# Performance work log

Hardware: AMD Instinct MI355X
Metric: run time of the kernel (lower is better)

## Reference

```python
import jax, jax.numpy as jnp
import numpy as np

S = 8192      # total patch tokens
NSEG = 8      # number of images/segments (equal length)
D = 1280      # embed dim
H = 16        # heads
HD = 80       # head dim
MLP = 3456    # swiglu hidden


def setup_inputs() -> dict:
    key = jax.random.key(0)
    ks = jax.random.split(key, 8)
    def w(k, shape):
        return jax.random.normal(k, shape, jnp.float32) * 0.02
    return {
        "x": jax.random.normal(ks[0], (S, 1, D), jnp.float32),
        "rotary_pos_emb": jax.random.uniform(ks[1], (S, HD // 2), jnp.float32) * 6.2831853,
        "cu_seqlens": jnp.arange(NSEG + 1, dtype=jnp.int32) * (S // NSEG),
        "norm1_w": jnp.ones((D,), jnp.float32), "norm1_b": jnp.zeros((D,), jnp.float32),
        "norm2_w": jnp.ones((D,), jnp.float32), "norm2_b": jnp.zeros((D,), jnp.float32),
        "w_qkv": w(ks[2], (3 * D, D)), "b_qkv": jnp.zeros((3 * D,), jnp.float32),
        "w_proj": w(ks[3], (D, D)), "b_proj": jnp.zeros((D,), jnp.float32),
        "w_gate": w(ks[4], (MLP, D)), "b_gate": jnp.zeros((MLP,), jnp.float32),
        "w_up": w(ks[5], (MLP, D)), "b_up": jnp.zeros((MLP,), jnp.float32),
        "w_down": w(ks[6], (D, MLP)), "b_down": jnp.zeros((D,), jnp.float32),
    }


def _ln(x, w, b, eps=1e-6):
    m = x.mean(-1, keepdims=True)
    v = ((x - m) ** 2).mean(-1, keepdims=True)
    return (x - m) * jax.lax.rsqrt(v + eps) * w + b


def _rope(x, cos, sin):
    # x: [B, S, H, HD]; cos/sin: [S, HD/2]; non-interleaved (chunk-halves) rotation
    c = jnp.concatenate([cos, cos], -1)[None, :, None, :]
    s = jnp.concatenate([sin, sin], -1)[None, :, None, :]
    x1, x2 = jnp.split(x, 2, -1)
    return x * c + jnp.concatenate([-x2, x1], -1) * s


def _forward(cu, x, freqs, norm1_w, norm1_b, norm2_w, norm2_b,
             w_qkv, b_qkv, w_proj, b_proj,
             w_gate, b_gate, w_up, b_up, w_down, b_down):
    S_, B, D_ = x.shape  # B == 1
    L = int(cu[1] - cu[0])          # equal-length segments
    nseg = len(cu) - 1
    h = _ln(x, norm1_w, norm1_b)
    qkv = h @ w_qkv.T + b_qkv                                   # [S, B, 3D]
    q, k, v = jnp.split(qkv, 3, -1)
    q, k, v = (t.reshape(S_, B, H, HD).transpose(1, 0, 2, 3) for t in (q, k, v))  # [B,S,H,d]
    cos, sin = jnp.cos(freqs), jnp.sin(freqs)
    q = _rope(q, cos, sin)
    k = _rope(k, cos, sin)
    # block-diagonal attention over cu_seqlens: fold segments into batch
    qs, ks_, vs = (t.reshape(B * nseg, L, H, HD) for t in (q, k, v))
    scale = 1.0 / np.float32(np.sqrt(HD))
    scores = jnp.einsum('blhd,bmhd->bhlm', qs, ks_) * scale     # [nseg,H,L,L]
    attn = jax.nn.softmax(scores, axis=-1)
    ctx = jnp.einsum('bhlm,bmhd->blhd', attn, vs)               # [nseg,L,H,d]
    ctx = ctx.reshape(B, S_, H * HD).transpose(1, 0, 2)         # [S,B,D]
    x = x + ctx @ w_proj.T + b_proj
    h2 = _ln(x, norm2_w, norm2_b)
    gate = jax.nn.silu(h2 @ w_gate.T + b_gate)
    up = h2 @ w_up.T + b_up
    return x + (gate * up) @ w_down.T + b_down


def reference(x, rotary_pos_emb, cu_seqlens, norm1_w, norm1_b, norm2_w, norm2_b,
              w_qkv, b_qkv, w_proj, b_proj, w_gate, b_gate, w_up, b_up,
              w_down, b_down):
    cu = np.asarray(cu_seqlens)
    return _forward(cu, x, rotary_pos_emb, norm1_w, norm1_b, norm2_w, norm2_b,
                    w_qkv, b_qkv, w_proj, b_proj,
                    w_gate, b_gate, w_up, b_up, w_down, b_down)
```

## Files before the change

### kernel.cpp

```cpp
#include <hip/hip_runtime.h>


#define S_TOK 8192
#define DIM   1280
#define NHEAD 16
#define HDIM  80
#define SEGLEN 1024
#define MLPD  3456

typedef __attribute__((ext_vector_type(8))) short bf16x8;
typedef __attribute__((ext_vector_type(8))) unsigned short u16x8;
typedef __attribute__((ext_vector_type(4))) float f32x4;

__device__ __forceinline__ float bf2f(unsigned short u) {
    unsigned int x = ((unsigned int)u) << 16;
    return __builtin_bit_cast(float, x);
}
__device__ __forceinline__ unsigned short f2bf(float f) {
    unsigned int x = __builtin_bit_cast(unsigned int, f);
    unsigned int r = x + 0x7fffu + ((x >> 16) & 1u);
    return (unsigned short)(r >> 16);
}

__device__ __forceinline__ void gload_lds16(const void* g, void* l) {
    __builtin_amdgcn_global_load_lds(
        (const __attribute__((address_space(1))) void*)g,
        (__attribute__((address_space(3))) void*)l, 16, 0, 0);
}

__device__ __forceinline__ int xcd_swz(int bid, int nwg) {
    const int q = nwg >> 3, r = nwg & 7;
    const int x = bid & 7, j = bid >> 3;
    return (x < r ? x * (q + 1) : r * (q + 1) + (x - r) * q) + j;
}

__global__ __launch_bounds__(256)
void f2b_kernel(const float* __restrict__ in, unsigned short* __restrict__ out, int n4)
{
    const int i = blockIdx.x * 256 + threadIdx.x;
    if (i >= n4) return;
    const float4 v = ((const float4*)in)[i];
    ushort4 o;
    o.x = f2bf(v.x); o.y = f2bf(v.y); o.z = f2bf(v.z); o.w = f2bf(v.w);
    ((ushort4*)out)[i] = o;
}

__global__ __launch_bounds__(256)
void ln_kernel(const float* __restrict__ xin,
               const float* __restrict__ w,
               const float* __restrict__ b,
               unsigned short* __restrict__ out)
{
    const int row = blockIdx.x;
    const int t = threadIdx.x;
    const size_t base = (size_t)row * DIM;
    float v[5];
#pragma unroll
    for (int i = 0; i < 5; ++i) v[i] = xin[base + t + i * 256];
    float s = 0.f, s2 = 0.f;
#pragma unroll
    for (int i = 0; i < 5; ++i) { s += v[i]; s2 += v[i] * v[i]; }
#pragma unroll
    for (int off = 32; off > 0; off >>= 1) {
        s  += __shfl_down(s, off);
        s2 += __shfl_down(s2, off);
    }
    __shared__ float rs[8];
    const int wave = t >> 6, lane = t & 63;
    if (lane == 0) { rs[wave] = s; rs[wave + 4] = s2; }
    __syncthreads();
    s  = rs[0] + rs[1] + rs[2] + rs[3];
    s2 = rs[4] + rs[5] + rs[6] + rs[7];
    const float mean = s * (1.f / DIM);
    const float var  = s2 * (1.f / DIM) - mean * mean;
    const float rstd = rsqrtf(var + 1e-6f);
#pragma unroll
    for (int i = 0; i < 5; ++i) {
        const int c = t + i * 256;
        out[base + c] = f2bf((v[i] - mean) * rstd * w[c] + b[c]);
    }
}

__global__ __launch_bounds__(256)
void rope_kernel(const unsigned short* __restrict__ qkv,
                 const float* __restrict__ rot,
                 unsigned short* __restrict__ qr,
                 unsigned short* __restrict__ kr)
{
    const int idx = blockIdx.x * 256 + threadIdx.x;
    const int s = idx / DIM, rem = idx % DIM;
    const int h = rem / HDIM, d = rem % HDIM;
    const int dd = (d < 40) ? d : d - 40;
    const float th = rot[s * 40 + dd];
    const float c = __cosf(th), sn = __sinf(th);
    const size_t base = (size_t)s * (3 * DIM) + h * HDIM;
    const int partner = (d < 40) ? d + 40 : d - 40;
    const float sgn = (d < 40) ? -1.f : 1.f;
    const float q  = bf2f(qkv[base + d]);
    const float k  = bf2f(qkv[DIM + base + d]);
    const float qp = bf2f(qkv[base + partner]);
    const float kp = bf2f(qkv[DIM + base + partner]);
    const float qo = q * c + sgn * qp * sn;
    const float ko = k * c + sgn * kp * sn;
    qr[idx] = f2bf(qo * 0.11180339887498949f);
    kr[idx] = f2bf(ko);
}

enum { EPI_BF16 = 0, EPI_RES = 1, EPI_GU = 2 };

template<int EPI, int BNV>
__global__ __launch_bounds__(512, 2)
void gemm4q(const unsigned short* __restrict__ A,
            const unsigned short* __restrict__ B0,
            const unsigned short* __restrict__ B1,
            const float* __restrict__ bias0,
            const float* __restrict__ bias1,
            void* __restrict__ C,
            const void* __restrict__ aux,
            int M, int N, int K, int ntn)
{
    constexpr int NF = BNV / 64;
    constexpr int BSLOT = BNV * 64;
    extern __shared__ __align__(16) unsigned short lds[];
    const int t = threadIdx.x;
    const int w = t >> 6, lane = t & 63;
    const int m = lane & 15, g = lane >> 4;
    const int wm = w >> 2, wn = w & 3;
    const int wg = xcd_swz(blockIdx.x, gridDim.x);
    const int nblk = wg % ntn;
    const int m0 = (wg / ntn) * 256;
    const int NT = K >> 6;

    f32x4 acc[8][NF] = {};

    auto STAGE_A = [&](int tt) {
        const int k0 = tt << 6;
        unsigned short* dst = lds + (tt & 1) * 16384;
#pragma unroll
        for (int i = 0; i < 4; ++i) {
            const int ch = i * 512 + t;
            const int row = ch >> 3, c = ch & 7;
            gload_lds16(A + (size_t)(m0 + row) * K + k0 + (c ^ (row & 7)) * 8,
                        dst + ch * 8);
        }
    };
    auto STAGE_B = [&](int tt) {
        const int k0 = tt << 6;
        unsigned short* dst = lds + 32768 + (tt & 1) * BSLOT;
#pragma unroll
        for (int i = 0; i < BNV / 64; ++i) {
            const int ch = i * 512 + t;
            const int row = ch >> 3, c = ch & 7;
            const unsigned short* src;
            if (EPI == EPI_GU) {
                src = (row < 128)
                    ? B0 + (size_t)(nblk * 128 + row) * K
                    : B1 + (size_t)(nblk * 128 + (row - 128)) * K;
            } else {
                src = B0 + (size_t)(nblk * BNV + row) * K;
            }
            gload_lds16(src + k0 + (c ^ (row & 7)) * 8, dst + ch * 8);
        }
    };

    STAGE_A(0); STAGE_B(0);
    asm volatile("s_waitcnt vmcnt(0)" ::: "memory");
    __builtin_amdgcn_s_barrier();

    for (int tt = 0; tt < NT; ++tt) {
        const unsigned short* As = lds + (tt & 1) * 16384;
        const unsigned short* Bs = lds + 32768 + (tt & 1) * BSLOT;
        bf16x8 bfr[NF];
#pragma unroll
        for (int kk = 0; kk < 2; ++kk) {
#pragma unroll
            for (int mh = 0; mh < 2; ++mh) {
                bf16x8 afr[4];
                const int cs = ((kk * 4 + g) ^ (m & 7)) * 8;
#pragma unroll
                for (int mf4 = 0; mf4 < 4; ++mf4) {
                    const int row = wm * 128 + (mh * 4 + mf4) * 16 + m;
                    afr[mf4] = *(const bf16x8*)&As[row * 64 + cs];
                }
                if (mh == 0) {
#pragma unroll
                    for (int nf = 0; nf < NF; ++nf) {
                        int rowb;
                        if (EPI == EPI_GU)
                            rowb = (nf < 2) ? (wn * 32 + nf * 16 + m)
                                            : (128 + wn * 32 + (nf - 2) * 16 + m);
                        else
                            rowb = wn * (BNV / 4) + nf * 16 + m;
                        bfr[nf] = *(const bf16x8*)&Bs[rowb * 64 + cs];
                    }
                }
                if (kk == 0 && mh == 0 && tt + 1 < NT) STAGE_A(tt + 1);
                if (kk == 0 && mh == 1 && tt + 1 < NT) STAGE_B(tt + 1);
                if (kk == 1 && mh == 1)
                    asm volatile("s_waitcnt vmcnt(0)" ::: "memory");
                __builtin_amdgcn_s_barrier();
                __builtin_amdgcn_s_setprio(1);
#pragma unroll
                for (int mf4 = 0; mf4 < 4; ++mf4)
#pragma unroll
                    for (int nf = 0; nf < NF; ++nf)
                        acc[mh * 4 + mf4][nf] = __builtin_amdgcn_mfma_f32_16x16x32_bf16(
                            afr[mf4], bfr[nf], acc[mh * 4 + mf4][nf], 0, 0, 0);
                __builtin_amdgcn_s_setprio(0);
                __builtin_amdgcn_s_barrier();
            }
        }
    }

#pragma unroll
    for (int mf = 0; mf < 8; ++mf) {
        const int row = m0 + wm * 128 + mf * 16 + g * 4;
        if (EPI == EPI_GU) {
#pragma unroll
            for (int nfp = 0; nfp < 2; ++nfp) {
                const int col = nblk * 128 + wn * 32 + nfp * 16 + m;
                const float bgv = bias0[col], buv = bias1[col];
#pragma unroll
                for (int i = 0; i < 4; ++i) {
                    const float gv = acc[mf][nfp][i] + bgv;
                    const float uv = acc[mf][nfp + 2][i] + buv;
                    const float sg = gv / (1.f + __expf(-gv));
                    ((unsigned short*)C)[(size_t)(row + i) * N + col] = f2bf(sg * uv);
                }
            }
        } else {
#pragma unroll
            for (int nf = 0; nf < NF; ++nf) {
                const int col = nblk * BNV + wn * (BNV / 4) + nf * 16 + m;
                const float bv = bias0[col];
#pragma unroll
                for (int i = 0; i < 4; ++i) {
                    const float v = acc[mf][nf][i] + bv;
                    const size_t idx = (size_t)(row + i) * N + col;
                    if (EPI == EPI_BF16) {
                        ((unsigned short*)C)[idx] = f2bf(v);
                    } else {
                        const float xr = ((const float*)aux)[idx];
                        ((float*)C)[idx] = v + xr;
                    }
                }
            }
        }
    }
}

__global__ __launch_bounds__(256)
void attn_mfma_kernel(const unsigned short* __restrict__ qr,
                      const unsigned short* __restrict__ kr,
                      const unsigned short* __restrict__ qkv,
                      unsigned short* __restrict__ ctx)
{
    const int qt = blockIdx.x, hh = blockIdx.y, seg = blockIdx.z;
    const int t = threadIdx.x;
    const int w = t >> 6, lane = t & 63;
    const int m = lane & 15, g = lane >> 4;

    __shared__ __align__(16) unsigned short Ks[64 * 80];
    __shared__ __align__(16) unsigned short Vt[80 * 72];
    __shared__ __align__(16) unsigned short Ps[4][16 * 72];

    const int q0 = seg * SEGLEN + qt * 64 + w * 16;

    bf16x8 qa0, qa1, qa2 = {};
    {
        const unsigned short* qrow = qr + (size_t)(q0 + m) * DIM + hh * HDIM;
        qa0 = *(const bf16x8*)(qrow + 8 * g);
        qa1 = *(const bf16x8*)(qrow + 32 + 8 * g);
        if (g < 2) qa2 = *(const bf16x8*)(qrow + 64 + 8 * g);
    }

    f32x4 o[5] = {};
    float mrow[4], lrow[4];
#pragma unroll
    for (int i = 0; i < 4; ++i) { mrow[i] = -1e30f; lrow[i] = 0.f; }

    for (int kt = 0; kt < SEGLEN / 64; ++kt) {
        const int kbase = seg * SEGLEN + kt * 64;
#pragma unroll
        for (int i = 0; i < 2; ++i) {
            const int ch = t + 256 * i;
            const int row = ch / 10, c = ch % 10;
            gload_lds16(kr + (size_t)(kbase + row) * DIM + hh * HDIM + c * 8,
                        &Ks[ch * 8]);
        }
        if (t < 128) {
            const int ch = 512 + t;
            const int row = ch / 10, c = ch % 10;
            gload_lds16(kr + (size_t)(kbase + row) * DIM + hh * HDIM + c * 8,
                        &Ks[ch * 8]);
        }
#pragma unroll
        for (int i = 0; i < 3; ++i) {
            const int ch = t + 256 * i;
            if (ch < 640) {
                const int k = ch & 63, dc = ch >> 6;
                const u16x8 v = *(const u16x8*)(qkv +
                    (size_t)(kbase + k) * (3 * DIM) + 2 * DIM + hh * HDIM + dc * 8);
#pragma unroll
                for (int e = 0; e < 8; ++e)
                    Vt[(dc * 8 + e) * 72 + k] = v[e];
            }
        }
        __syncthreads();

        f32x4 s[4] = {};
#pragma unroll
        for (int nn = 0; nn < 4; ++nn) {
            const unsigned short* kb = &Ks[(16 * nn + m) * 80];
            const bf16x8 b0 = *(const bf16x8*)(kb + 8 * g);
            const bf16x8 b1 = *(const bf16x8*)(kb + 32 + 8 * g);
            bf16x8 b2 = {};
            if (g < 2) b2 = *(const bf16x8*)(kb + 64 + 8 * g);
            s[nn] = __builtin_amdgcn_mfma_f32_16x16x32_bf16(qa0, b0, s[nn], 0, 0, 0);
            s[nn] = __builtin_amdgcn_mfma_f32_16x16x32_bf16(qa1, b1, s[nn], 0, 0, 0);
            s[nn] = __builtin_amdgcn_mfma_f32_16x16x32_bf16(qa2, b2, s[nn], 0, 0, 0);
        }

#pragma unroll
        for (int i = 0; i < 4; ++i) {
            float mx = fmaxf(fmaxf(s[0][i], s[1][i]), fmaxf(s[2][i], s[3][i]));
            mx = fmaxf(mx, __shfl_xor(mx, 1));
            mx = fmaxf(mx, __shfl_xor(mx, 2));
            mx = fmaxf(mx, __shfl_xor(mx, 4));
            mx = fmaxf(mx, __shfl_xor(mx, 8));
            const float mn = fmaxf(mrow[i], mx);
            const float fs = __expf(mrow[i] - mn);
            float rs = 0.f;
#pragma unroll
            for (int nn = 0; nn < 4; ++nn) {
                const float p = __expf(s[nn][i] - mn);
                s[nn][i] = p;
                rs += p;
            }
            rs += __shfl_xor(rs, 1);
            rs += __shfl_xor(rs, 2);
            rs += __shfl_xor(rs, 4);
            rs += __shfl_xor(rs, 8);
            lrow[i] = lrow[i] * fs + rs;
            mrow[i] = mn;
#pragma unroll
            for (int df = 0; df < 5; ++df) o[df][i] *= fs;
        }

#pragma unroll
        for (int nn = 0; nn < 4; ++nn)
#pragma unroll
            for (int i = 0; i < 4; ++i)
                Ps[w][(4 * g + i) * 72 + 16 * nn + m] = f2bf(s[nn][i]);

        const bf16x8 pa0 = *(const bf16x8*)&Ps[w][m * 72 + 8 * g];
        const bf16x8 pa1 = *(const bf16x8*)&Ps[w][m * 72 + 32 + 8 * g];
#pragma unroll
        for (int df = 0; df < 5; ++df) {
            const unsigned short* vb = &Vt[(16 * df + m) * 72];
            const bf16x8 vb0 = *(const bf16x8*)(vb + 8 * g);
            const bf16x8 vb1 = *(const bf16x8*)(vb + 32 + 8 * g);
            o[df] = __builtin_amdgcn_mfma_f32_16x16x32_bf16(pa0, vb0, o[df], 0, 0, 0);
            o[df] = __builtin_amdgcn_mfma_f32_16x16x32_bf16(pa1, vb1, o[df], 0, 0, 0);
        }
        __syncthreads();
    }

#pragma unroll
    for (int i = 0; i < 4; ++i) {
        const float inv = 1.f / lrow[i];
        unsigned short* crow = ctx + (size_t)(q0 + 4 * g + i) * DIM + hh * HDIM;
#pragma unroll
        for (int df = 0; df < 5; ++df)
            crow[16 * df + m] = f2bf(o[df][i] * inv);
    }
}

extern "C" void kernel_launch(void* const* d_in, const int* in_sizes, int n_in,
                              void* d_out, int out_size, void* d_ws, size_t ws_size,
                              hipStream_t stream)
{
    const float* x      = (const float*)d_in[0];
    const float* rot    = (const float*)d_in[1];
    const float* n1w    = (const float*)d_in[3];
    const float* n1b    = (const float*)d_in[4];
    const float* n2w    = (const float*)d_in[5];
    const float* n2b    = (const float*)d_in[6];
    const float* w_qkv  = (const float*)d_in[7];
    const float* b_qkv  = (const float*)d_in[8];
    const float* w_proj = (const float*)d_in[9];
    const float* b_proj = (const float*)d_in[10];
    const float* w_gate = (const float*)d_in[11];
    const float* b_gate = (const float*)d_in[12];
    const float* w_up   = (const float*)d_in[13];
    const float* b_up   = (const float*)d_in[14];
    const float* w_down = (const float*)d_in[15];
    const float* b_down = (const float*)d_in[16];

    char* ws = (char*)d_ws;
    unsigned short* qkv  = (unsigned short*)(ws + 0);
    unsigned short* h    = (unsigned short*)(ws + 62914560ull);
    unsigned short* qr   = (unsigned short*)(ws + 83886080ull);
    unsigned short* kr   = (unsigned short*)(ws + 104857600ull);
    unsigned short* ctx  = (unsigned short*)(ws + 125829120ull);
    float*          x2   = (float*)(ws + 146800640ull);
    unsigned short* wqb  = (unsigned short*)(ws + 188743680ull);
    unsigned short* wpb  = (unsigned short*)(ws + 198574080ull);
    unsigned short* wgb  = (unsigned short*)(ws + 201850880ull);
    unsigned short* wub  = (unsigned short*)(ws + 210698240ull);
    unsigned short* wdb  = (unsigned short*)(ws + 219545600ull);
    unsigned short* gbuf = qkv;

    hipFuncSetAttribute(reinterpret_cast<const void*>(gemm4q<EPI_BF16, 256>),
                        hipFuncAttributeMaxDynamicSharedMemorySize, 131072);
    hipFuncSetAttribute(reinterpret_cast<const void*>(gemm4q<EPI_GU, 256>),
                        hipFuncAttributeMaxDynamicSharedMemorySize, 131072);
    hipFuncSetAttribute(reinterpret_cast<const void*>(gemm4q<EPI_RES, 128>),
                        hipFuncAttributeMaxDynamicSharedMemorySize, 98304);

    {
        const int nq = 3 * DIM * DIM / 4, np = DIM * DIM / 4, nm = MLPD * DIM / 4;
        f2b_kernel<<<(nq + 255) / 256, 256, 0, stream>>>(w_qkv,  wqb, nq);
        f2b_kernel<<<(np + 255) / 256, 256, 0, stream>>>(w_proj, wpb, np);
        f2b_kernel<<<(nm + 255) / 256, 256, 0, stream>>>(w_gate, wgb, nm);
        f2b_kernel<<<(nm + 255) / 256, 256, 0, stream>>>(w_up,   wub, nm);
        f2b_kernel<<<(nm + 255) / 256, 256, 0, stream>>>(w_down, wdb, nm);
    }

    ln_kernel<<<S_TOK, 256, 0, stream>>>(x, n1w, n1b, h);
    gemm4q<EPI_BF16, 256><<<15 * 32, 512, 131072, stream>>>(
        h, wqb, nullptr, b_qkv, nullptr, qkv, nullptr, S_TOK, 3 * DIM, DIM, 15);
    rope_kernel<<<(S_TOK * DIM) / 256, 256, 0, stream>>>(qkv, rot, qr, kr);
    attn_mfma_kernel<<<dim3(SEGLEN / 64, NHEAD, S_TOK / SEGLEN), 256, 0, stream>>>(
        qr, kr, qkv, ctx);
    gemm4q<EPI_RES, 128><<<10 * 32, 512, 98304, stream>>>(
        ctx, wpb, nullptr, b_proj, nullptr, x2, x, S_TOK, DIM, DIM, 10);
    ln_kernel<<<S_TOK, 256, 0, stream>>>(x2, n2w, n2b, h);
    gemm4q<EPI_GU, 256><<<27 * 32, 512, 131072, stream>>>(
        h, wgb, wub, b_gate, b_up, gbuf, nullptr, S_TOK, MLPD, DIM, 27);
    gemm4q<EPI_RES, 128><<<10 * 32, 512, 98304, stream>>>(
        gbuf, wdb, nullptr, b_down, nullptr, (float*)d_out, x2, S_TOK, DIM, MLPD, 10);
}
```

Before: 653.5 us.

## Split-K the down projection GEMM and vectorize the RoPE kernel

The down-projection GEMM (K=3456) now runs as a 3-way split-K with 256-wide N tiles, giving 480 workgroups instead of 320. Each split writes fp32 partials, one into the output buffer and two into workspace, and a separate reduce kernel adds the partials, the residual and the bias. The RoPE kernel now has each thread handle 8 consecutive dims of both halves with 16-byte vector loads and stores instead of one scalar element. The split-K adds roughly 120MB of extra fp32 partial traffic and one more launch in exchange for better CU occupancy.

```diff
diff --git a/kernel.cpp b/kernel.cpp
--- a/kernel.cpp
+++ b/kernel.cpp
@@ -87,26 +87,39 @@
                  unsigned short* __restrict__ qr,
                  unsigned short* __restrict__ kr)
 {
-    const int idx = blockIdx.x * 256 + threadIdx.x;
-    const int s = idx / DIM, rem = idx % DIM;
-    const int h = rem / HDIM, d = rem % HDIM;
-    const int dd = (d < 40) ? d : d - 40;
-    const float th = rot[s * 40 + dd];
-    const float c = __cosf(th), sn = __sinf(th);
-    const size_t base = (size_t)s * (3 * DIM) + h * HDIM;
-    const int partner = (d < 40) ? d + 40 : d - 40;
-    const float sgn = (d < 40) ? -1.f : 1.f;
-    const float q  = bf2f(qkv[base + d]);
-    const float k  = bf2f(qkv[DIM + base + d]);
-    const float qp = bf2f(qkv[base + partner]);
-    const float kp = bf2f(qkv[DIM + base + partner]);
-    const float qo = q * c + sgn * qp * sn;
-    const float ko = k * c + sgn * kp * sn;
-    qr[idx] = f2bf(qo * 0.11180339887498949f);
-    kr[idx] = f2bf(ko);
-}
-
-enum { EPI_BF16 = 0, EPI_RES = 1, EPI_GU = 2 };
+    const int i = blockIdx.x * 256 + threadIdx.x;
+    const int s = i / 80, r = i % 80;
+    const int h = r / 5, d0 = (r % 5) * 8;
+    const unsigned short* qp = qkv + (size_t)s * (3 * DIM) + h * HDIM;
+    const unsigned short* kp = qp + DIM;
+    const u16x8 qlo = *(const u16x8*)(qp + d0);
+    const u16x8 qhi = *(const u16x8*)(qp + 40 + d0);
+    const u16x8 klo = *(const u16x8*)(kp + d0);
+    const u16x8 khi = *(const u16x8*)(kp + 40 + d0);
+    const float4 r0 = *(const float4*)(rot + s * 40 + d0);
+    const float4 r1 = *(const float4*)(rot + s * 40 + d0 + 4);
+    u16x8 qlo_o, qhi_o, klo_o, khi_o;
+    const float sc = 0.11180339887498949f;
+#pragma unroll
+    for (int j = 0; j < 8; ++j) {
+        const float th = (j < 4) ? ((const float*)&r0)[j] : ((const float*)&r1)[j - 4];
+        const float c = __cosf(th), sn = __sinf(th);
+        const float ql = bf2f(qlo[j]), qh = bf2f(qhi[j]);
+        const float kl = bf2f(klo[j]), kh = bf2f(khi[j]);
+        qlo_o[j] = f2bf((ql * c - qh * sn) * sc);
+        qhi_o[j] = f2bf((qh * c + ql * sn) * sc);
+        klo_o[j] = f2bf(kl * c - kh * sn);
+        khi_o[j] = f2bf(kh * c + kl * sn);
+    }
+    unsigned short* qo = qr + (size_t)s * DIM + h * HDIM;
+    unsigned short* ko = kr + (size_t)s * DIM + h * HDIM;
+    *(u16x8*)(qo + d0) = qlo_o;
+    *(u16x8*)(qo + 40 + d0) = qhi_o;
+    *(u16x8*)(ko + d0) = klo_o;
+    *(u16x8*)(ko + 40 + d0) = khi_o;
+}
+
+enum { EPI_BF16 = 0, EPI_RES = 1, EPI_GU = 2, EPI_PART = 3 };
 
 template<int EPI, int BNV>
 __global__ __launch_bounds__(512, 2)
@@ -117,7 +130,7 @@
             const float* __restrict__ bias1,
             void* __restrict__ C,
             const void* __restrict__ aux,
-            int M, int N, int K, int ntn)
+            int M, int N, int K, int ntn, int ktps)
 {
     constexpr int NF = BNV / 64;
     constexpr int BSLOT = BNV * 64;
@@ -127,9 +140,12 @@
     const int m = lane & 15, g = lane >> 4;
     const int wm = w >> 2, wn = w & 3;
     const int wg = xcd_swz(blockIdx.x, gridDim.x);
-    const int nblk = wg % ntn;
-    const int m0 = (wg / ntn) * 256;
-    const int NT = K >> 6;
+    const int per = ntn * (M >> 8);
+    const int split = wg / per;
+    const int rem = wg % per;
+    const int nblk = rem % ntn;
+    const int m0 = (rem / ntn) * 256;
+    const int tbeg = split * ktps, tend = tbeg + ktps;
 
     f32x4 acc[8][NF] = {};
 
@@ -163,11 +179,11 @@
         }
     };
 
-    STAGE_A(0); STAGE_B(0);
+    STAGE_A(tbeg); STAGE_B(tbeg);
     asm volatile("s_waitcnt vmcnt(0)" ::: "memory");
     __builtin_amdgcn_s_barrier();
 
-    for (int tt = 0; tt < NT; ++tt) {
+    for (int tt = tbeg; tt < tend; ++tt) {
         const unsigned short* As = lds + (tt & 1) * 16384;
         const unsigned short* Bs = lds + 32768 + (tt & 1) * BSLOT;
         bf16x8 bfr[NF];
@@ -194,8 +210,8 @@
                         bfr[nf] = *(const bf16x8*)&Bs[rowb * 64 + cs];
                     }
                 }
-                if (kk == 0 && mh == 0 && tt + 1 < NT) STAGE_A(tt + 1);
-                if (kk == 0 && mh == 1 && tt + 1 < NT) STAGE_B(tt + 1);
+                if (kk == 0 && mh == 0 && tt + 1 < tend) STAGE_A(tt + 1);
+                if (kk == 0 && mh == 1 && tt + 1 < tend) STAGE_B(tt + 1);
                 if (kk == 1 && mh == 1)
                     asm volatile("s_waitcnt vmcnt(0)" ::: "memory");
                 __builtin_amdgcn_s_barrier();
@@ -227,6 +243,17 @@
                     const float sg = gv / (1.f + __expf(-gv));
                     ((unsigned short*)C)[(size_t)(row + i) * N + col] = f2bf(sg * uv);
                 }
+            }
+        } else if (EPI == EPI_PART) {
+            float* Cp = (split == 0)
+                ? (float*)C
+                : (float*)aux + (size_t)(split - 1) * M * N;
+#pragma unroll
+            for (int nf = 0; nf < NF; ++nf) {
+                const int col = nblk * BNV + wn * (BNV / 4) + nf * 16 + m;
+#pragma unroll
+                for (int i = 0; i < 4; ++i)
+                    Cp[(size_t)(row + i) * N + col] = acc[mf][nf][i];
             }
         } else {
 #pragma unroll
@@ -247,6 +274,26 @@
             }
         }
     }
+}
+
+__global__ __launch_bounds__(256)
+void reduce_down(const float* __restrict__ p0, const float* __restrict__ p1,
+                 const float* __restrict__ p2, const float* __restrict__ x2,
+                 const float* __restrict__ bias, float* __restrict__ out)
+{
+    const int i = blockIdx.x * 256 + threadIdx.x;
+    const int col = (i * 4) % DIM;
+    const float4 a = ((const float4*)p0)[i];
+    const float4 b = ((const float4*)p1)[i];
+    const float4 c = ((const float4*)p2)[i];
+    const float4 d = ((const float4*)x2)[i];
+    const float4 bv = *(const float4*)(bias + col);
+    float4 o;
+    o.x = a.x + b.x + c.x + d.x + bv.x;
+    o.y = a.y + b.y + c.y + d.y + bv.y;
+    o.z = a.z + b.z + c.z + d.z + bv.z;
+    o.w = a.w + b.w + c.w + d.w + bv.w;
+    ((float4*)out)[i] = o;
 }
 
 __global__ __launch_bounds__(256)
@@ -410,6 +457,7 @@
     unsigned short* wub  = (unsigned short*)(ws + 210698240ull);
     unsigned short* wdb  = (unsigned short*)(ws + 219545600ull);
     unsigned short* gbuf = qkv;
+    float* dparts = (float*)(ws + 62914560ull);
 
     hipFuncSetAttribute(reinterpret_cast<const void*>(gemm4q<EPI_BF16, 256>),
                         hipFuncAttributeMaxDynamicSharedMemorySize, 131072);
@@ -417,6 +465,8 @@
                         hipFuncAttributeMaxDynamicSharedMemorySize, 131072);
     hipFuncSetAttribute(reinterpret_cast<const void*>(gemm4q<EPI_RES, 128>),
                         hipFuncAttributeMaxDynamicSharedMemorySize, 98304);
+    hipFuncSetAttribute(reinterpret_cast<const void*>(gemm4q<EPI_PART, 256>),
+                        hipFuncAttributeMaxDynamicSharedMemorySize, 131072);
 
     {
         const int nq = 3 * DIM * DIM / 4, np = DIM * DIM / 4, nm = MLPD * DIM / 4;
@@ -429,15 +479,22 @@
 
     ln_kernel<<<S_TOK, 256, 0, stream>>>(x, n1w, n1b, h);
     gemm4q<EPI_BF16, 256><<<15 * 32, 512, 131072, stream>>>(
-        h, wqb, nullptr, b_qkv, nullptr, qkv, nullptr, S_TOK, 3 * DIM, DIM, 15);
-    rope_kernel<<<(S_TOK * DIM) / 256, 256, 0, stream>>>(qkv, rot, qr, kr);
+        h, wqb, nullptr, b_qkv, nullptr, qkv, nullptr,
+        S_TOK, 3 * DIM, DIM, 15, DIM / 64);
+    rope_kernel<<<(S_TOK * 80) / 256, 256, 0, stream>>>(qkv, rot, qr, kr);
     attn_mfma_kernel<<<dim3(SEGLEN / 64, NHEAD, S_TOK / SEGLEN), 256, 0, stream>>>(
         qr, kr, qkv, ctx);
     gemm4q<EPI_RES, 128><<<10 * 32, 512, 98304, stream>>>(
-        ctx, wpb, nullptr, b_proj, nullptr, x2, x, S_TOK, DIM, DIM, 10);
+        ctx, wpb, nullptr, b_proj, nullptr, x2, x,
+        S_TOK, DIM, DIM, 10, DIM / 64);
     ln_kernel<<<S_TOK, 256, 0, stream>>>(x2, n2w, n2b, h);
     gemm4q<EPI_GU, 256><<<27 * 32, 512, 131072, stream>>>(
-        h, wgb, wub, b_gate, b_up, gbuf, nullptr, S_TOK, MLPD, DIM, 27);
-    gemm4q<EPI_RES, 128><<<10 * 32, 512, 98304, stream>>>(
-        gbuf, wdb, nullptr, b_down, nullptr, (float*)d_out, x2, S_TOK, DIM, MLPD, 10);
-}
+        h, wgb, wub, b_gate, b_up, gbuf, nullptr,
+        S_TOK, MLPD, DIM, 27, DIM / 64);
+    gemm4q<EPI_PART, 256><<<3 * 5 * 32, 512, 131072, stream>>>(
+        gbuf, wdb, nullptr, nullptr, nullptr, (float*)d_out, dparts,
+        S_TOK, DIM, MLPD, 5, 18);
+    reduce_down<<<(S_TOK * DIM / 4) / 256, 256, 0, stream>>>(
+        (const float*)d_out, dparts, dparts + (size_t)S_TOK * DIM,
+        x2, b_down, (float*)d_out);
+}
```

After: 644.8 us. No clear change (-1.3%).
